# Optimization experiments

Measured on AMD Instinct MI355X. Metric: run time of the kernel, lower is better.

Reference implementation:

```python
import jax, jax.numpy as jnp
import numpy as np

N, E = 50000, 400000
HID, EDIM, H, FFN_MULT = 128, 32, 2, 2
C = HID  # out_channels per head (PyG TransformerConv out_channels)


def _layernorm(x, g, b, eps=1e-5):
    mu = jnp.mean(x, axis=-1, keepdims=True)
    var = jnp.mean(jnp.square(x - mu), axis=-1, keepdims=True)
    return (x - mu) * jax.lax.rsqrt(var + eps) * g + b


def setup_inputs() -> dict:
    key = jax.random.key(0)
    ks = jax.random.split(key, 16)
    s = 0.05
    inp = {
        "x": jax.random.normal(ks[0], (N, HID), jnp.float32),
        "edge_index": jax.random.randint(ks[1], (2, E), 0, N, jnp.int64),
        "edge_attr": jax.random.normal(ks[2], (E, EDIM), jnp.float32),
        # TransformerConv projections (lin_query/key/value: bias=True; lin_edge: bias=False; lin_skip: bias=True)
        "Wq": jax.random.normal(ks[3], (H * C, HID), jnp.float32) * s,
        "bq": jnp.zeros((H * C,), jnp.float32),
        "Wk": jax.random.normal(ks[4], (H * C, HID), jnp.float32) * s,
        "bk": jnp.zeros((H * C,), jnp.float32),
        "Wv": jax.random.normal(ks[5], (H * C, HID), jnp.float32) * s,
        "bv": jnp.zeros((H * C,), jnp.float32),
        "We": jax.random.normal(ks[6], (H * C, EDIM), jnp.float32) * s,
        "Wskip": jax.random.normal(ks[7], (HID, HID), jnp.float32) * s,
        "bskip": jnp.zeros((HID,), jnp.float32),
        "ln1_g": jnp.ones((HID,), jnp.float32),
        "ln1_b": jnp.zeros((HID,), jnp.float32),
        "W1": jax.random.normal(ks[8], (HID * FFN_MULT, HID), jnp.float32) * s,
        "b1": jnp.zeros((HID * FFN_MULT,), jnp.float32),
        "W2": jax.random.normal(ks[9], (HID, HID * FFN_MULT), jnp.float32) * s,
        "b2": jnp.zeros((HID,), jnp.float32),
        "ln2_g": jnp.ones((HID,), jnp.float32),
        "ln2_b": jnp.zeros((HID,), jnp.float32),
    }
    return inp


def reference(x, edge_index, edge_attr, Wq, bq, Wk, bk, Wv, bv, We, Wskip, bskip,
              ln1_g, ln1_b, W1, b1, W2, b2, ln2_g, ln2_b):
    n = x.shape[0]
    src, dst = edge_index[0], edge_index[1]  # messages flow src -> dst
    q = (x @ Wq.T + bq).reshape(n, H, C)
    k = (x @ Wk.T + bk).reshape(n, H, C)
    v = (x @ Wv.T + bv).reshape(n, H, C)
    e = (edge_attr @ We.T).reshape(-1, H, C)  # [E,H,C]
    k_j = k[src] + e
    alpha = jnp.sum(q[dst] * k_j, axis=-1) / jnp.sqrt(jnp.float32(C))  # [E,H]
    # segment-wise (per-destination-node) softmax, numerically stable
    amax = jax.ops.segment_max(alpha, dst, num_segments=n)
    amax = jnp.where(jnp.isfinite(amax), amax, 0.0)
    ex = jnp.exp(alpha - amax[dst])
    denom = jax.ops.segment_sum(ex, dst, num_segments=n)
    w = ex / (denom[dst] + 1e-16)  # [E,H]
    msg = (v[src] + e) * w[:, :, None]  # [E,H,C]
    agg = jax.ops.segment_sum(msg, dst, num_segments=n)  # [N,H,C]
    out = jnp.mean(agg, axis=1)  # concat=False -> mean over heads
    attn_out = out + x @ Wskip.T + bskip  # root_weight skip
    # block: residual + LN, FFN, residual + LN (dropout = identity at inference)
    h = _layernorm(x + attn_out, ln1_g, ln1_b)
    f = jax.nn.leaky_relu(h @ W1.T + b1, negative_slope=0.01) @ W2.T + b2
    return _layernorm(h + f, ln2_g, ln2_b)
```

## Files before the change

### kernel.cpp

```cpp
#include <hip/hip_runtime.h>
#include <hip/hip_bf16.h>


typedef __attribute__((ext_vector_type(8))) short bf16x8;
typedef __attribute__((ext_vector_type(8))) unsigned short u16x8;
typedef __attribute__((ext_vector_type(4))) float f32x4;

__device__ __forceinline__ float bf2f(unsigned short u) {
    union { float f; unsigned u32; } x; x.u32 = ((unsigned)u) << 16; return x.f;
}
__device__ __forceinline__ unsigned short f2bf(float f) {
    unsigned u = __float_as_uint(f);
    return (unsigned short)((u + 0x7FFFu + ((u >> 16) & 1u)) >> 16);
}

template<int ACT, int EPI, int OUT_BF16, int AF32>
__global__ __launch_bounds__(256)
void gemm_fused(const void* __restrict__ Ap, int lda,
                const unsigned short* __restrict__ W, int ldw,
                const float* __restrict__ bias,
                void* __restrict__ outp, int ldo, int M, int K,
                const float* __restrict__ add0, const float* __restrict__ add1,
                const unsigned short* __restrict__ skipp, int skip_ld,
                const unsigned short* __restrict__ hprev,
                const float* __restrict__ lng, const float* __restrict__ lnb) {
    __shared__ unsigned short As[128 * 40];
    __shared__ unsigned short Bs[128 * 40];
    const int tid = threadIdx.x;
    const int wave = tid >> 6, lane = tid & 63;

    int row0, col0;
    {
        const int gx   = gridDim.x;
        const int nwg  = gx * gridDim.y;
        const int orig = blockIdx.y * gx + blockIdx.x;
        const int q8   = nwg >> 3, r8 = nwg & 7;
        const int xcd  = orig & 7, sub = orig >> 3;
        const int swz  = (xcd < r8 ? xcd * (q8 + 1)
                                   : r8 * (q8 + 1) + (xcd - r8) * q8) + sub;
        row0 = (swz / gx) * 128;
        col0 = (swz % gx) * 128;
    }

    const int srow = tid >> 2;
    const int skg  = (tid & 3) * 8;
    int r0 = row0 + srow;      if (r0 >= M) r0 = 0;
    int r1 = row0 + srow + 64; if (r1 >= M) r1 = 0;
    const int b0 = col0 + srow, b1 = col0 + srow + 64;

    f32x4 acc[2][8];
    const f32x4 z4 = {0.f, 0.f, 0.f, 0.f};
    #pragma unroll
    for (int i = 0; i < 2; i++)
        #pragma unroll
        for (int j = 0; j < 8; j++) acc[i][j] = z4;

    const int mrow = wave * 32 + (lane & 15);
    const int kq = (lane >> 4) * 8;

    for (int kt = 0; kt < K; kt += 32) {
        u16x8 a0v, a1v;
        if (AF32) {
            const float* Af = (const float*)Ap;
            float4 xa = *(const float4*)(Af + (size_t)r0 * lda + kt + skg);
            float4 xb = *(const float4*)(Af + (size_t)r0 * lda + kt + skg + 4);
            float4 ya = *(const float4*)(Af + (size_t)r1 * lda + kt + skg);
            float4 yb = *(const float4*)(Af + (size_t)r1 * lda + kt + skg + 4);
            a0v[0]=f2bf(xa.x); a0v[1]=f2bf(xa.y); a0v[2]=f2bf(xa.z); a0v[3]=f2bf(xa.w);
            a0v[4]=f2bf(xb.x); a0v[5]=f2bf(xb.y); a0v[6]=f2bf(xb.z); a0v[7]=f2bf(xb.w);
            a1v[0]=f2bf(ya.x); a1v[1]=f2bf(ya.y); a1v[2]=f2bf(ya.z); a1v[3]=f2bf(ya.w);
            a1v[4]=f2bf(yb.x); a1v[5]=f2bf(yb.y); a1v[6]=f2bf(yb.z); a1v[7]=f2bf(yb.w);
        } else {
            const unsigned short* Ah = (const unsigned short*)Ap;
            a0v = *(const u16x8*)(Ah + (size_t)r0 * lda + kt + skg);
            a1v = *(const u16x8*)(Ah + (size_t)r1 * lda + kt + skg);
        }
        float4 w0 = *(const float4*)(W + (size_t)b0 * ldw + kt + skg);
        float4 w1 = *(const float4*)(W + (size_t)b1 * ldw + kt + skg);
        __syncthreads();
        *(u16x8*)&As[srow * 40 + skg]        = a0v;
        *(u16x8*)&As[(srow + 64) * 40 + skg] = a1v;
        *(float4*)&Bs[srow * 40 + skg]        = w0;
        *(float4*)&Bs[(srow + 64) * 40 + skg] = w1;
        __syncthreads();
        bf16x8 af0 = *(const bf16x8*)&As[mrow * 40 + kq];
        bf16x8 af1 = *(const bf16x8*)&As[(mrow + 16) * 40 + kq];
        bf16x8 bfr[8];
        #pragma unroll
        for (int j = 0; j < 8; j++)
            bfr[j] = *(const bf16x8*)&Bs[(j * 16 + (lane & 15)) * 40 + kq];
        #pragma unroll
        for (int j = 0; j < 8; j++) {
            acc[0][j] = __builtin_amdgcn_mfma_f32_16x16x32_bf16(af0, bfr[j], acc[0][j], 0, 0, 0);
            acc[1][j] = __builtin_amdgcn_mfma_f32_16x16x32_bf16(af1, bfr[j], acc[1][j], 0, 0, 0);
        }
    }

    const int lgrp = lane & 15;
    if (EPI == 0) {
        const int orow0 = row0 + wave * 32 + ((lane >> 4) << 2);
        const int ocol0 = col0 + lgrp;
        #pragma unroll
        for (int i = 0; i < 2; i++) {
            #pragma unroll
            for (int r = 0; r < 4; r++) {
                int row = orow0 + i * 16 + r;
                if (row >= M) continue;
                #pragma unroll
                for (int j = 0; j < 8; j++) {
                    int col = ocol0 + j * 16;
                    float v = acc[i][j][r] + (bias ? bias[col] : 0.f);
                    if (ACT == 1) v = (v > 0.f) ? v : 0.01f * v;
                    if (OUT_BF16) ((unsigned short*)outp)[(size_t)row * ldo + col] = f2bf(v);
                    else          ((float*)outp)[(size_t)row * ldo + col] = v;
                }
            }
        }
    } else {
        #pragma unroll
        for (int i = 0; i < 2; i++) {
            #pragma unroll
            for (int r = 0; r < 4; r++) {
                int row = row0 + wave * 32 + ((lane >> 4) << 2) + i * 16 + r;
                if (row >= M) continue;
                float t[8];
                #pragma unroll
                for (int j = 0; j < 8; j++) {
                    int col = lgrp + j * 16;
                    float v = acc[i][j][r];
                    if (EPI == 1) {
                        v += add0[(size_t)row * 128 + col] + add1[(size_t)row * 128 + col]
                           + bf2f(skipp[(size_t)row * skip_ld + col]);
                    } else {
                        v += bias[col];
                        v += bf2f(hprev[(size_t)row * 128 + col]);
                    }
                    t[j] = v;
                }
                float s = 0.f;
                #pragma unroll
                for (int j = 0; j < 8; j++) s += t[j];
                #pragma unroll
                for (int off = 8; off >= 1; off >>= 1) s += __shfl_xor(s, off);
                float mu = s * (1.f / 128.f);
                float q = 0.f;
                #pragma unroll
                for (int j = 0; j < 8; j++) { float d = t[j] - mu; q += d * d; }
                #pragma unroll
                for (int off = 8; off >= 1; off >>= 1) q += __shfl_xor(q, off);
                float rs = rsqrtf(q * (1.f / 128.f) + 1e-5f);
                #pragma unroll
                for (int j = 0; j < 8; j++) {
                    int col = lgrp + j * 16;
                    float o = (t[j] - mu) * rs * lng[col] + lnb[col];
                    if (EPI == 1) ((unsigned short*)outp)[(size_t)row * ldo + col] = f2bf(o);
                    else          ((float*)outp)[(size_t)row * ldo + col] = o;
                }
            }
        }
    }
}

#define WPREP 205824
__global__ void prep_all(const float* __restrict__ Wq, const float* __restrict__ bq,
                         const float* __restrict__ Wk, const float* __restrict__ bk,
                         const float* __restrict__ Wv, const float* __restrict__ bv,
                         const float* __restrict__ We, const float* __restrict__ Wsk,
                         const float* __restrict__ bsk,
                         const float* __restrict__ W1, const float* __restrict__ W2,
                         unsigned short* __restrict__ Wcat, float* __restrict__ bcat,
                         unsigned short* __restrict__ W1h, unsigned short* __restrict__ W2h,
                         unsigned short* __restrict__ Wec2,
                         const int* __restrict__ dst, int* __restrict__ deg, int E) {
    int k = blockIdx.x * 256 + threadIdx.x;
    if (k >= WPREP) {
        int e = k - WPREP;
        if (e < E) atomicAdd(&deg[dst[e]], 1);
        return;
    }
    if (k < 131072) {
        int oc = k >> 7, r = k & 127;
        float v;
        if (oc < 256) v = Wq[(size_t)oc * 128 + r];
        else if (oc < 768) {
            int rr = oc - 256, g = rr >> 3, p = rr & 7;
            int h = g >> 5, ch = h * 128 + (g & 31) * 4 + (p & 3);
            v = (p < 4) ? Wk[(size_t)ch * 128 + r] : Wv[(size_t)ch * 128 + r];
        } else if (oc < 896) v = Wsk[(size_t)(oc - 768) * 128 + r];
        else if (oc < 960) {
            int qd = oc - 896, h = qd >> 5, t = qd & 31;
            float s = 0.f;
            for (int c = 0; c < 128; c++)
                s += Wq[(size_t)(h*128 + c) * 128 + r] * We[(size_t)(h*128 + c) * 32 + t];
            v = s;
        } else v = 0.f;
        Wcat[k] = f2bf(v);
    } else if (k < 132096) {
        int oc = k - 131072;
        float v;
        if (oc < 256) v = bq[oc];
        else if (oc < 768) {
            int rr = oc - 256, g = rr >> 3, p = rr & 7;
            int ch = (g >> 5) * 128 + (g & 31) * 4 + (p & 3);
            v = (p < 4) ? bk[ch] : bv[ch];
        } else if (oc < 896) v = bsk[oc - 768];
        else if (oc < 960) {
            int qd = oc - 896, h = qd >> 5, t = qd & 31;
            float s = 0.f;
            for (int c = 0; c < 128; c++)
                s += bq[h*128 + c] * We[(size_t)(h*128 + c) * 32 + t];
            v = s;
        } else v = 0.f;
        bcat[oc] = v;
    } else if (k < 164864) {
        int j = k - 132096;
        W1h[j] = f2bf(W1[j]);
    } else if (k < 197632) {
        int j = k - 164864;
        W2h[j] = f2bf(W2[j]);
    } else {
        int j = k - 197632;
        int c = j >> 6, tt = j & 63, h = tt >> 5, t = tt & 31;
        Wec2[j] = f2bf(0.5f * We[(size_t)(h * 128 + c) * 32 + t]);
    }
}

__global__ __launch_bounds__(256)
void scan_block(const int* __restrict__ deg, int* __restrict__ tmp,
                int* __restrict__ bsum, int n) {
    __shared__ int lds[256];
    int i = blockIdx.x * 256 + threadIdx.x;
    int v = (i < n) ? deg[i] : 0;
    lds[threadIdx.x] = v;
    __syncthreads();
    #pragma unroll
    for (int off = 1; off < 256; off <<= 1) {
        int t = (threadIdx.x >= off) ? lds[threadIdx.x - off] : 0;
        __syncthreads();
        lds[threadIdx.x] += t;
        __syncthreads();
    }
    if (i < n) tmp[i] = lds[threadIdx.x];
    if (threadIdx.x == 255) bsum[blockIdx.x] = lds[255];
}
__global__ __launch_bounds__(1024)
void scan_bsum(int* __restrict__ bsum, int nb) {
    __shared__ int lds[1024];
    int v = (threadIdx.x < nb) ? bsum[threadIdx.x] : 0;
    lds[threadIdx.x] = v;
    __syncthreads();
    #pragma unroll
    for (int off = 1; off < 1024; off <<= 1) {
        int t = (threadIdx.x >= off) ? lds[threadIdx.x - off] : 0;
        __syncthreads();
        lds[threadIdx.x] += t;
        __syncthreads();
    }
    if (threadIdx.x < nb) bsum[threadIdx.x] = lds[threadIdx.x] - v;
}
__global__ void csr_fill(const int* __restrict__ src, const int* __restrict__ dst,
                         const int* __restrict__ tmp, const int* __restrict__ sbx,
                         int* __restrict__ cnt, int2* __restrict__ eid2, int E) {
    int e = blockIdx.x * blockDim.x + threadIdx.x;
    if (e < E) {
        int d = dst[e];
        int start = (d == 0) ? 0 : (tmp[d - 1] + sbx[(d - 1) >> 8]);
        int pos = start + atomicAdd(&cnt[d], 1);
        eid2[pos] = make_int2(e, src[e]);
    }
}

__global__ __launch_bounds__(64)
void fused_attn(const unsigned short* __restrict__ O1, const float* __restrict__ EA,
                const int* __restrict__ tmp, const int* __restrict__ sbx,
                const int2* __restrict__ eid2,
                float* __restrict__ agg, unsigned short* __restrict__ weab, int N) {
    const int node = blockIdx.x;
    const int lane = threadIdx.x;
    const int hl = lane & 31;
    const int choff = (lane >> 5) * 128 + (hl << 2);
    const float inv = 0.08838834764831845f;

    ushort4 q4 = *(const ushort4*)(O1 + (size_t)node * 1024 + choff);
    float4 qv = make_float4(bf2f(q4.x), bf2f(q4.y), bf2f(q4.z), bf2f(q4.w));
    float pd = bf2f(O1[(size_t)node * 1024 + 896 + lane]);

    const int j0 = (node == 0) ? 0 : (tmp[node - 1] + sbx[(node - 1) >> 8]);
    const int jend = tmp[node] + sbx[node >> 8];

    float l = 0.f, wacc = 0.f;
    float4 acc = make_float4(0.f, 0.f, 0.f, 0.f);

    const u16x8 zkv = {0,0,0,0,0,0,0,0};
    u16x8 kvA0, kvA1, kvB0, kvB1;
    float eaA0, eaA1, eaB0, eaB1;
    int2 es0, es1;

    int j = j0;
    if (j < jend) {
        {
            int2 es = eid2[j];
            kvA0 = *(const u16x8*)(O1 + (size_t)es.y * 1024 + 256 + lane * 8);
            eaA0 = EA[(size_t)es.x * 32 + hl];
        }
        if (j + 1 < jend) {
            int2 es = eid2[j + 1];
            kvA1 = *(const u16x8*)(O1 + (size_t)es.y * 1024 + 256 + lane * 8);
            eaA1 = EA[(size_t)es.x * 32 + hl];
        } else { kvA1 = zkv; eaA1 = 0.f; }
        es0 = (j + 2 < jend) ? eid2[j + 2] : make_int2(0, -1);
        es1 = (j + 3 < jend) ? eid2[j + 3] : make_int2(0, -1);

        while (j < jend) {
            if (es0.y >= 0) {
                kvB0 = *(const u16x8*)(O1 + (size_t)es0.y * 1024 + 256 + lane * 8);
                eaB0 = EA[(size_t)es0.x * 32 + hl];
            } else { kvB0 = zkv; eaB0 = 0.f; }
            if (es1.y >= 0) {
                kvB1 = *(const u16x8*)(O1 + (size_t)es1.y * 1024 + 256 + lane * 8);
                eaB1 = EA[(size_t)es1.x * 32 + hl];
            } else { kvB1 = zkv; eaB1 = 0.f; }
            es0 = (j + 4 < jend) ? eid2[j + 4] : make_int2(0, -1);
            es1 = (j + 5 < jend) ? eid2[j + 5] : make_int2(0, -1);
            {
                float d0 = qv.x*bf2f(kvA0[0]) + qv.y*bf2f(kvA0[1])
                         + qv.z*bf2f(kvA0[2]) + qv.w*bf2f(kvA0[3]) + pd*eaA0;
                float d1 = qv.x*bf2f(kvA1[0]) + qv.y*bf2f(kvA1[1])
                         + qv.z*bf2f(kvA1[2]) + qv.w*bf2f(kvA1[3]) + pd*eaA1;
                #pragma unroll
                for (int off = 16; off >= 1; off >>= 1) {
                    d0 += __shfl_xor(d0, off);
                    d1 += __shfl_xor(d1, off);
                }
                float w0 = __expf(d0 * inv);
                float w1 = (j + 1 < jend) ? __expf(d1 * inv) : 0.f;
                l += w0 + w1;
                acc.x += w0*bf2f(kvA0[4]) + w1*bf2f(kvA1[4]);
                acc.y += w0*bf2f(kvA0[5]) + w1*bf2f(kvA1[5]);
                acc.z += w0*bf2f(kvA0[6]) + w1*bf2f(kvA1[6]);
                acc.w += w0*bf2f(kvA0[7]) + w1*bf2f(kvA1[7]);
                wacc  += w0*eaA0 + w1*eaA1;
            }
            j += 2;
            if (j >= jend) break;

            if (es0.y >= 0) {
                kvA0 = *(const u16x8*)(O1 + (size_t)es0.y * 1024 + 256 + lane * 8);
                eaA0 = EA[(size_t)es0.x * 32 + hl];
            } else { kvA0 = zkv; eaA0 = 0.f; }
            if (es1.y >= 0) {
                kvA1 = *(const u16x8*)(O1 + (size_t)es1.y * 1024 + 256 + lane * 8);
                eaA1 = EA[(size_t)es1.x * 32 + hl];
            } else { kvA1 = zkv; eaA1 = 0.f; }
            es0 = (j + 4 < jend) ? eid2[j + 4] : make_int2(0, -1);
            es1 = (j + 5 < jend) ? eid2[j + 5] : make_int2(0, -1);
            {
                float d0 = qv.x*bf2f(kvB0[0]) + qv.y*bf2f(kvB0[1])
                         + qv.z*bf2f(kvB0[2]) + qv.w*bf2f(kvB0[3]) + pd*eaB0;
                float d1 = qv.x*bf2f(kvB1[0]) + qv.y*bf2f(kvB1[1])
                         + qv.z*bf2f(kvB1[2]) + qv.w*bf2f(kvB1[3]) + pd*eaB1;
                #pragma unroll
                for (int off = 16; off >= 1; off >>= 1) {
                    d0 += __shfl_xor(d0, off);
                    d1 += __shfl_xor(d1, off);
                }
                float w0 = __expf(d0 * inv);
                float w1 = (j + 1 < jend) ? __expf(d1 * inv) : 0.f;
                l += w0 + w1;
                acc.x += w0*bf2f(kvB0[4]) + w1*bf2f(kvB1[4]);
                acc.y += w0*bf2f(kvB0[5]) + w1*bf2f(kvB1[5]);
                acc.z += w0*bf2f(kvB0[6]) + w1*bf2f(kvB1[6]);
                acc.w += w0*bf2f(kvB0[7]) + w1*bf2f(kvB1[7]);
                wacc  += w0*eaB0 + w1*eaB1;
            }
            j += 2;
        }
    }

    float r = 1.f / (l + 1e-16f);
    weab[(size_t)node * 64 + lane] = f2bf(wacc * r);
    float ax = acc.x * r, ay = acc.y * r, az = acc.z * r, aw = acc.w * r;
    float mx = 0.5f * (ax + __shfl_xor(ax, 32));
    float my = 0.5f * (ay + __shfl_xor(ay, 32));
    float mz = 0.5f * (az + __shfl_xor(az, 32));
    float mw = 0.5f * (aw + __shfl_xor(aw, 32));
    if (lane < 32)
        *(float4*)(agg + (size_t)node * 128 + hl * 4) = make_float4(mx, my, mz, mw);
}

extern "C" void kernel_launch(void* const* d_in, const int* in_sizes, int n_in,
                              void* d_out, int out_size, void* d_ws, size_t ws_size,
                              hipStream_t stream) {
    const float* x    = (const float*)d_in[0];
    const int*   ei   = (const int*)d_in[1];
    const float* ea   = (const float*)d_in[2];
    const float* Wq   = (const float*)d_in[3];
    const float* bq   = (const float*)d_in[4];
    const float* Wk   = (const float*)d_in[5];
    const float* bk   = (const float*)d_in[6];
    const float* Wv   = (const float*)d_in[7];
    const float* bv   = (const float*)d_in[8];
    const float* We   = (const float*)d_in[9];
    const float* Wsk  = (const float*)d_in[10];
    const float* bsk  = (const float*)d_in[11];
    const float* g1   = (const float*)d_in[12];
    const float* b1l  = (const float*)d_in[13];
    const float* W1   = (const float*)d_in[14];
    const float* b1f  = (const float*)d_in[15];
    const float* W2   = (const float*)d_in[16];
    const float* b2f  = (const float*)d_in[17];
    const float* g2   = (const float*)d_in[18];
    const float* b2l  = (const float*)d_in[19];
    float* out = (float*)d_out;

    const int N = in_sizes[0] / 128;
    const int E = in_sizes[2] / 32;
    const int* src = ei;
    const int* dst = ei + E;

    char* w = (char*)d_ws;
    unsigned short* O1   = (unsigned short*)w;  w += (size_t)N * 2048;
    float* agg           = (float*)w;           w += (size_t)N * 512;
    unsigned short* weab = (unsigned short*)w;  w += (size_t)N * 128;
    unsigned short* hb   = (unsigned short*)w;  w += (size_t)N * 256;
    unsigned short* Wcat = (unsigned short*)w;  w += 1024 * 128 * 2;
    float* bcat          = (float*)w;           w += 1024 * 4;
    unsigned short* W1h  = (unsigned short*)w;  w += 256 * 128 * 2;
    unsigned short* W2h  = (unsigned short*)w;  w += 128 * 256 * 2;
    unsigned short* Wec2 = (unsigned short*)w;  w += 128 * 64 * 2;
    int2* eid2           = (int2*)w;            w += (size_t)E * 8;
    int* deg  = (int*)w;
    int* cnt  = deg + N;
    int* tmp  = cnt + N;
    int* bsum = tmp + N;

    unsigned short* mid = (unsigned short*)agg;

    const int gy128 = (N + 127) / 128;
    const int nb = (N + 255) / 256;

    hipMemsetAsync(deg, 0, (size_t)2 * N * 4, stream);
    prep_all<<<(WPREP + E + 255) / 256, 256, 0, stream>>>(
        Wq, bq, Wk, bk, Wv, bv, We, Wsk, bsk, W1, W2,
        Wcat, bcat, W1h, W2h, Wec2, dst, deg, E);

    gemm_fused<0,0,1,1><<<dim3(8, gy128), 256, 0, stream>>>(
        x, 128, Wcat, 128, bcat, O1, 1024, N, 128,
        nullptr, nullptr, nullptr, 0, nullptr, nullptr, nullptr);

    scan_block<<<nb, 256, 0, stream>>>(deg, tmp, bsum, N);
    scan_bsum<<<1, 1024, 0, stream>>>(bsum, nb);
    csr_fill<<<(E + 255)/256, 256, 0, stream>>>(src, dst, tmp, bsum, cnt, eid2, E);

    fused_attn<<<N, 64, 0, stream>>>(O1, ea, tmp, bsum, eid2, agg, weab, N);

    gemm_fused<0,1,1,0><<<dim3(1, gy128), 256, 0, stream>>>(
        weab, 64, Wec2, 64, nullptr, hb, 128, N, 64,
        agg, x, O1 + 768, 1024, nullptr, g1, b1l);

    gemm_fused<1,0,1,0><<<dim3(2, gy128), 256, 0, stream>>>(
        hb, 128, W1h, 128, b1f, mid, 256, N, 128,
        nullptr, nullptr, nullptr, 0, nullptr, nullptr, nullptr);

    gemm_fused<0,2,0,0><<<dim3(1, gy128), 256, 0, stream>>>(
        mid, 256, W2h, 256, b2f, out, 128, N, 256,
        nullptr, nullptr, nullptr, 0, hb, g2, b2l);
}
```

Baseline: 391.9 us.

## Batch GEMM K-chunk loads into multi-chunk LDS passes with compile-time K

Makes K a template parameter and stages up to four 32-wide K chunks per pass. All global loads for a pass are issued together, written to a larger LDS buffer, and then consumed with one pair of barriers instead of two per chunk. This is meant to expose more memory-level parallelism and cut synchronization overhead in the small-K GEMMs. In exchange it raises register pressure and LDS use (up to about 80KB per block), which may lower occupancy.

```diff
diff --git a/kernel.cpp b/kernel.cpp
--- a/kernel.cpp
+++ b/kernel.cpp
@@ -14,18 +14,23 @@
     return (unsigned short)((u + 0x7FFFu + ((u >> 16) & 1u)) >> 16);
 }
 
-template<int ACT, int EPI, int OUT_BF16, int AF32>
+template<int ACT, int EPI, int OUT_BF16, int AF32, int K>
 __global__ __launch_bounds__(256)
 void gemm_fused(const void* __restrict__ Ap, int lda,
                 const unsigned short* __restrict__ W, int ldw,
                 const float* __restrict__ bias,
-                void* __restrict__ outp, int ldo, int M, int K,
+                void* __restrict__ outp, int ldo, int M,
                 const float* __restrict__ add0, const float* __restrict__ add1,
                 const unsigned short* __restrict__ skipp, int skip_ld,
                 const unsigned short* __restrict__ hprev,
                 const float* __restrict__ lng, const float* __restrict__ lnb) {
-    __shared__ unsigned short As[128 * 40];
-    __shared__ unsigned short Bs[128 * 40];
+    constexpr int NCH   = K / 32;
+    constexpr int CPP   = (NCH < 4) ? NCH : 4;
+    constexpr int NPASS = NCH / CPP;
+    constexpr int CH    = 128 * 40;
+    __shared__ unsigned short As[CPP * CH];
+    __shared__ unsigned short Bs[CPP * CH];
+
     const int tid = threadIdx.x;
     const int wave = tid >> 6, lane = tid & 63;
 
@@ -58,41 +63,52 @@
     const int mrow = wave * 32 + (lane & 15);
     const int kq = (lane >> 4) * 8;
 
-    for (int kt = 0; kt < K; kt += 32) {
-        u16x8 a0v, a1v;
-        if (AF32) {
-            const float* Af = (const float*)Ap;
-            float4 xa = *(const float4*)(Af + (size_t)r0 * lda + kt + skg);
-            float4 xb = *(const float4*)(Af + (size_t)r0 * lda + kt + skg + 4);
-            float4 ya = *(const float4*)(Af + (size_t)r1 * lda + kt + skg);
-            float4 yb = *(const float4*)(Af + (size_t)r1 * lda + kt + skg + 4);
-            a0v[0]=f2bf(xa.x); a0v[1]=f2bf(xa.y); a0v[2]=f2bf(xa.z); a0v[3]=f2bf(xa.w);
-            a0v[4]=f2bf(xb.x); a0v[5]=f2bf(xb.y); a0v[6]=f2bf(xb.z); a0v[7]=f2bf(xb.w);
-            a1v[0]=f2bf(ya.x); a1v[1]=f2bf(ya.y); a1v[2]=f2bf(ya.z); a1v[3]=f2bf(ya.w);
-            a1v[4]=f2bf(yb.x); a1v[5]=f2bf(yb.y); a1v[6]=f2bf(yb.z); a1v[7]=f2bf(yb.w);
-        } else {
-            const unsigned short* Ah = (const unsigned short*)Ap;
-            a0v = *(const u16x8*)(Ah + (size_t)r0 * lda + kt + skg);
-            a1v = *(const u16x8*)(Ah + (size_t)r1 * lda + kt + skg);
-        }
-        float4 w0 = *(const float4*)(W + (size_t)b0 * ldw + kt + skg);
-        float4 w1 = *(const float4*)(W + (size_t)b1 * ldw + kt + skg);
-        __syncthreads();
-        *(u16x8*)&As[srow * 40 + skg]        = a0v;
-        *(u16x8*)&As[(srow + 64) * 40 + skg] = a1v;
-        *(float4*)&Bs[srow * 40 + skg]        = w0;
-        *(float4*)&Bs[(srow + 64) * 40 + skg] = w1;
-        __syncthreads();
-        bf16x8 af0 = *(const bf16x8*)&As[mrow * 40 + kq];
-        bf16x8 af1 = *(const bf16x8*)&As[(mrow + 16) * 40 + kq];
-        bf16x8 bfr[8];
-        #pragma unroll
-        for (int j = 0; j < 8; j++)
-            bfr[j] = *(const bf16x8*)&Bs[(j * 16 + (lane & 15)) * 40 + kq];
-        #pragma unroll
-        for (int j = 0; j < 8; j++) {
-            acc[0][j] = __builtin_amdgcn_mfma_f32_16x16x32_bf16(af0, bfr[j], acc[0][j], 0, 0, 0);
-            acc[1][j] = __builtin_amdgcn_mfma_f32_16x16x32_bf16(af1, bfr[j], acc[1][j], 0, 0, 0);
+    for (int ps = 0; ps < NPASS; ps++) {
+        u16x8 sa0[CPP], sa1[CPP];
+        float4 sw0[CPP], sw1[CPP];
+        #pragma unroll
+        for (int c = 0; c < CPP; c++) {
+            const int kt = (ps * CPP + c) * 32;
+            if (AF32) {
+                const float* Af = (const float*)Ap;
+                float4 xa = *(const float4*)(Af + (size_t)r0 * lda + kt + skg);
+                float4 xb = *(const float4*)(Af + (size_t)r0 * lda + kt + skg + 4);
+                float4 ya = *(const float4*)(Af + (size_t)r1 * lda + kt + skg);
+                float4 yb = *(const float4*)(Af + (size_t)r1 * lda + kt + skg + 4);
+                sa0[c][0]=f2bf(xa.x); sa0[c][1]=f2bf(xa.y); sa0[c][2]=f2bf(xa.z); sa0[c][3]=f2bf(xa.w);
+                sa0[c][4]=f2bf(xb.x); sa0[c][5]=f2bf(xb.y); sa0[c][6]=f2bf(xb.z); sa0[c][7]=f2bf(xb.w);
+                sa1[c][0]=f2bf(ya.x); sa1[c][1]=f2bf(ya.y); sa1[c][2]=f2bf(ya.z); sa1[c][3]=f2bf(ya.w);
+                sa1[c][4]=f2bf(yb.x); sa1[c][5]=f2bf(yb.y); sa1[c][6]=f2bf(yb.z); sa1[c][7]=f2bf(yb.w);
+            } else {
+                const unsigned short* Ah = (const unsigned short*)Ap;
+                sa0[c] = *(const u16x8*)(Ah + (size_t)r0 * lda + kt + skg);
+                sa1[c] = *(const u16x8*)(Ah + (size_t)r1 * lda + kt + skg);
+            }
+            sw0[c] = *(const float4*)(W + (size_t)b0 * ldw + kt + skg);
+            sw1[c] = *(const float4*)(W + (size_t)b1 * ldw + kt + skg);
+        }
+        __syncthreads();
+        #pragma unroll
+        for (int c = 0; c < CPP; c++) {
+            *(u16x8*)&As[c * CH + srow * 40 + skg]         = sa0[c];
+            *(u16x8*)&As[c * CH + (srow + 64) * 40 + skg]  = sa1[c];
+            *(float4*)&Bs[c * CH + srow * 40 + skg]        = sw0[c];
+            *(float4*)&Bs[c * CH + (srow + 64) * 40 + skg] = sw1[c];
+        }
+        __syncthreads();
+        #pragma unroll
+        for (int c = 0; c < CPP; c++) {
+            bf16x8 af0 = *(const bf16x8*)&As[c * CH + mrow * 40 + kq];
+            bf16x8 af1 = *(const bf16x8*)&As[c * CH + (mrow + 16) * 40 + kq];
+            bf16x8 bfr[8];
+            #pragma unroll
+            for (int j = 0; j < 8; j++)
+                bfr[j] = *(const bf16x8*)&Bs[c * CH + (j * 16 + (lane & 15)) * 40 + kq];
+            #pragma unroll
+            for (int j = 0; j < 8; j++) {
+                acc[0][j] = __builtin_amdgcn_mfma_f32_16x16x32_bf16(af0, bfr[j], acc[0][j], 0, 0, 0);
+                acc[1][j] = __builtin_amdgcn_mfma_f32_16x16x32_bf16(af1, bfr[j], acc[1][j], 0, 0, 0);
+            }
         }
     }
 
@@ -444,8 +460,8 @@
         Wq, bq, Wk, bk, Wv, bv, We, Wsk, bsk, W1, W2,
         Wcat, bcat, W1h, W2h, Wec2, dst, deg, E);
 
-    gemm_fused<0,0,1,1><<<dim3(8, gy128), 256, 0, stream>>>(
-        x, 128, Wcat, 128, bcat, O1, 1024, N, 128,
+    gemm_fused<0,0,1,1,128><<<dim3(8, gy128), 256, 0, stream>>>(
+        x, 128, Wcat, 128, bcat, O1, 1024, N,
         nullptr, nullptr, nullptr, 0, nullptr, nullptr, nullptr);
 
     scan_block<<<nb, 256, 0, stream>>>(deg, tmp, bsum, N);
@@ -454,15 +470,15 @@
 
     fused_attn<<<N, 64, 0, stream>>>(O1, ea, tmp, bsum, eid2, agg, weab, N);
 
-    gemm_fused<0,1,1,0><<<dim3(1, gy128), 256, 0, stream>>>(
-        weab, 64, Wec2, 64, nullptr, hb, 128, N, 64,
+    gemm_fused<0,1,1,0,64><<<dim3(1, gy128), 256, 0, stream>>>(
+        weab, 64, Wec2, 64, nullptr, hb, 128, N,
         agg, x, O1 + 768, 1024, nullptr, g1, b1l);
 
-    gemm_fused<1,0,1,0><<<dim3(2, gy128), 256, 0, stream>>>(
-        hb, 128, W1h, 128, b1f, mid, 256, N, 128,
+    gemm_fused<1,0,1,0,128><<<dim3(2, gy128), 256, 0, stream>>>(
+        hb, 128, W1h, 128, b1f, mid, 256, N,
         nullptr, nullptr, nullptr, 0, nullptr, nullptr, nullptr);
 
-    gemm_fused<0,2,0,0><<<dim3(1, gy128), 256, 0, stream>>>(
-        mid, 256, W2h, 256, b2f, out, 128, N, 256,
+    gemm_fused<0,2,0,0,256><<<dim3(1, gy128), 256, 0, stream>>>(
+        mid, 256, W2h, 256, b2f, out, 128, N,
         nullptr, nullptr, nullptr, 0, hb, g2, b2l);
 }
```

After: 448.1 us. 1.14x slower.
